# Optimization experiments

Measured on AMD Instinct MI355X. Metric: run time of the kernel, lower is better.

The kernel has to match this reference:

```python
import jax, jax.numpy as jnp
import numpy as np

N_NODES = 50000
N_EDGES = 800000
D_IN, D_HID, D_OUT = 128, 128, 256
EPS = 1e-12  # F.normalize eps


def _mean_aggr(h, src, dst, n):
    # scatter-mean of source features onto destination nodes
    msg_sum = jax.ops.segment_sum(h[src], dst, num_segments=n)
    deg = jax.ops.segment_sum(jnp.ones((src.shape[0],), h.dtype), dst, num_segments=n)
    return msg_sum / jnp.maximum(deg, 1.0)[:, None]


def _l2_normalize(h):
    # F.normalize(p=2, dim=1): divide by clamped L2 norm
    nrm = jnp.sqrt(jnp.sum(h * h, axis=1, keepdims=True))
    return h / jnp.maximum(nrm, EPS)


def setup_inputs() -> dict:
    key = jax.random.key(0)
    ks = jax.random.split(key, 8)
    x = jax.random.normal(ks[0], (N_NODES, D_IN), dtype=jnp.float32)
    edge_index = jax.random.randint(ks[1], (2, N_EDGES), 0, N_NODES, dtype=jnp.int64 if jax.config.read('jax_enable_x64') else jnp.int32)
    s = 1.0 / np.sqrt(D_IN)
    W1_l = jax.random.uniform(ks[2], (D_IN, D_HID), jnp.float32, -s, s)
    W1_r = jax.random.uniform(ks[3], (D_IN, D_HID), jnp.float32, -s, s)
    b1 = jnp.zeros((D_HID,), jnp.float32)
    s2 = 1.0 / np.sqrt(D_HID)
    W2_l = jax.random.uniform(ks[4], (D_HID, D_OUT), jnp.float32, -s2, s2)
    W2_r = jax.random.uniform(ks[5], (D_HID, D_OUT), jnp.float32, -s2, s2)
    b2 = jnp.zeros((D_OUT,), jnp.float32)
    return {"x": x, "edge_index": edge_index, "W1_l": W1_l, "W1_r": W1_r,
            "b1": b1, "W2_l": W2_l, "W2_r": W2_r, "b2": b2}


def reference(x, edge_index, W1_l, W1_r, b1, W2_l, W2_r, b2):
    src, dst = edge_index[0], edge_index[1]
    n = x.shape[0]
    # SAGEConv 1: lin_l(mean_aggr(x)) + lin_r(x) + bias
    h = _mean_aggr(x, src, dst, n) @ W1_l + x @ W1_r + b1
    # dropout is identity in eval mode
    h = _l2_normalize(jax.nn.sigmoid(h))
    # SAGEConv 2
    h = _mean_aggr(h, src, dst, n) @ W2_l + h @ W2_r + b2
    h = _l2_normalize(jax.nn.sigmoid(h))
    return jax.nn.log_softmax(h, axis=-1)
```

## Files before the change

### kernel.cpp

```cpp
#include <hip/hip_runtime.h>

#define NN 50000
#define NE 800000
#define NB 782
#define CAP 1536


__device__ __forceinline__ unsigned short f2bf(float f) {
    union { float f; unsigned u; } v; v.f = f;
    unsigned u = v.u;
    return (unsigned short)((u + 0x7fffu + ((u >> 16) & 1u)) >> 16);
}
__device__ __forceinline__ float bfu_lo(unsigned p) {
    union { unsigned u; float f; } v; v.u = p << 16; return v.f;
}
__device__ __forceinline__ float bfu_hi(unsigned p) {
    union { unsigned u; float f; } v; v.u = p & 0xffff0000u; return v.f;
}

typedef __bf16 bf16x8 __attribute__((ext_vector_type(8)));
typedef float f32x4 __attribute__((ext_vector_type(4)));
union U16 { uint4 u; bf16x8 v; };


__global__ __launch_bounds__(512) void binscatter_kernel(const int* __restrict__ src,
                                                         const int* __restrict__ dst,
                                                         int* __restrict__ bcnt,
                                                         unsigned* __restrict__ ebuf) {
    __shared__ int hist[NB];
    __shared__ int base[NB];
    const int BE = 8192;
    int tid = threadIdx.x;
    int e0 = blockIdx.x * BE;
    for (int i = tid; i < NB; i += 512) hist[i] = 0;
    __syncthreads();
    for (int i = tid; i < BE; i += 512) {
        int e = e0 + i;
        if (e < NE) atomicAdd(&hist[dst[e] >> 6], 1);
    }
    __syncthreads();
    for (int i = tid; i < NB; i += 512) {
        int c = hist[i];
        base[i] = c ? atomicAdd(&bcnt[i], c) : 0;
        hist[i] = 0;
    }
    __syncthreads();
    for (int i = tid; i < BE; i += 512) {
        int e = e0 + i;
        if (e < NE) {
            int d = dst[e], b = d >> 6;
            int slot = base[b] + atomicAdd(&hist[b], 1);
            if (slot < CAP)
                ebuf[(size_t)b * CAP + slot] = (unsigned)src[e] | ((unsigned)(d & 63) << 16);
        }
    }
}

__global__ __launch_bounds__(256) void csr_kernel(const int* __restrict__ bcnt,
                                                  const unsigned* __restrict__ ebuf,
                                                  int* __restrict__ rowptr,
                                                  int* __restrict__ col) {
    __shared__ int red[256];
    __shared__ int deg[64];
    __shared__ int cur[64];
    __shared__ int cbase_s;
    int b = blockIdx.x, tid = threadIdx.x;
    int s = 0;
    for (int i = tid; i < b; i += 256) s += bcnt[i];
    red[tid] = s;
    if (tid < 64) deg[tid] = 0;
    __syncthreads();
    for (int off = 128; off; off >>= 1) {
        if (tid < off) red[tid] += red[tid + off];
        __syncthreads();
    }
    if (tid == 0) cbase_s = red[0];
    __syncthreads();
    int cnt = bcnt[b], cbase = cbase_s;
    if (cnt > CAP) cnt = CAP;
    const unsigned* eb = ebuf + (size_t)b * CAP;
    for (int i = tid; i < cnt; i += 256) atomicAdd(&deg[(eb[i] >> 16) & 63], 1);
    __syncthreads();
    if (tid == 0) {
        int run = 0;
        for (int j = 0; j < 64; j++) { cur[j] = run; run += deg[j]; }
    }
    __syncthreads();
    int node = b * 64 + tid;
    if (tid < 64 && node < NN) rowptr[node] = cbase + cur[tid];
    if (b == NB - 1 && tid == 0) rowptr[NN] = NE;
    __syncthreads();
    for (int i = tid; i < cnt; i += 256) {
        unsigned e = eb[i];
        int pos = atomicAdd(&cur[(e >> 16) & 63], 1);
        col[cbase + pos] = (int)(e & 0xffffu);
    }
}


__global__ void cast_bf16_kernel(const float* __restrict__ in, unsigned short* __restrict__ outp,
                                 int n4) {
    int i = blockIdx.x * 256 + threadIdx.x;
    if (i < n4) {
        float4 f = ((const float4*)in)[i];
        ushort4 o;
        o.x = f2bf(f.x); o.y = f2bf(f.y); o.z = f2bf(f.z); o.w = f2bf(f.w);
        ((ushort4*)outp)[i] = o;
    }
}


template <int N>
__device__ __forceinline__ void pack_one(const float* __restrict__ Wl,
                                         const float* __restrict__ Wr,
                                         unsigned short* __restrict__ Wp, int t) {
    int lane = t & 63, c = t >> 6;
    int ks = c & 7, nt = c >> 3;
    int n = nt * 16 + (lane & 15);
    int kq = ks * 32 + (lane >> 4) * 8;
    unsigned short tmp[8];
#pragma unroll
    for (int j = 0; j < 8; j++) {
        int k = kq + j;
        float w = (k < 128) ? Wl[(size_t)k * N + n] : Wr[(size_t)(k - 128) * N + n];
        tmp[j] = f2bf(w);
    }
    ((ushort4*)Wp)[(size_t)c * 128 + lane * 2 + 0] = make_ushort4(tmp[0], tmp[1], tmp[2], tmp[3]);
    ((ushort4*)Wp)[(size_t)c * 128 + lane * 2 + 1] = make_ushort4(tmp[4], tmp[5], tmp[6], tmp[7]);
}

__global__ void pack_both_kernel(const float* __restrict__ W1l, const float* __restrict__ W1r,
                                 unsigned short* __restrict__ W1p,
                                 const float* __restrict__ W2l, const float* __restrict__ W2r,
                                 unsigned short* __restrict__ W2p) {
    int t = blockIdx.x * 256 + threadIdx.x;
    if (t < 8 * 8 * 64) pack_one<128>(W1l, W1r, W1p, t);
    else if (t < 8 * 8 * 64 + 16 * 8 * 64) pack_one<256>(W2l, W2r, W2p, t - 8 * 8 * 64);
}


__global__ void aggregate_bf_kernel(const int* __restrict__ rowptr, const int* __restrict__ col,
                                    const uint4* __restrict__ feat4,
                                    uint4* __restrict__ out4) {
    int wid = (blockIdx.x * blockDim.x + threadIdx.x) >> 6;
    int lane = threadIdx.x & 63;
    if (wid >= NN) return;
    int beg = rowptr[wid], end = rowptr[wid + 1];
    int g = lane >> 4, c16 = lane & 15;
    float acc[8];
#pragma unroll
    for (int j = 0; j < 8; j++) acc[j] = 0.f;
    for (int i = beg; i < end; i += 4) {
        int idx = i + g;
        if (idx < end) {
            int s = col[idx];
            uint4 v = feat4[(size_t)s * 16 + c16];
            acc[0] += bfu_lo(v.x); acc[1] += bfu_hi(v.x);
            acc[2] += bfu_lo(v.y); acc[3] += bfu_hi(v.y);
            acc[4] += bfu_lo(v.z); acc[5] += bfu_hi(v.z);
            acc[6] += bfu_lo(v.w); acc[7] += bfu_hi(v.w);
        }
    }
#pragma unroll
    for (int j = 0; j < 8; j++) {
        acc[j] += __shfl_xor(acc[j], 16);
        acc[j] += __shfl_xor(acc[j], 32);
    }
    if (g == 0) {
        float inv = (end > beg) ? 1.0f / (float)(end - beg) : 0.0f;
        uint4 o;
        o.x = (unsigned)f2bf(acc[0] * inv) | ((unsigned)f2bf(acc[1] * inv) << 16);
        o.y = (unsigned)f2bf(acc[2] * inv) | ((unsigned)f2bf(acc[3] * inv) << 16);
        o.z = (unsigned)f2bf(acc[4] * inv) | ((unsigned)f2bf(acc[5] * inv) << 16);
        o.w = (unsigned)f2bf(acc[6] * inv) | ((unsigned)f2bf(acc[7] * inv) << 16);
        out4[(size_t)wid * 16 + c16] = o;
    }
}


template <int N, bool FINAL>
__global__ __launch_bounds__(256) void gemm_mfma_kernel(
    const unsigned short* __restrict__ A0, const unsigned short* __restrict__ A1,
    const unsigned short* __restrict__ Wp, const float* __restrict__ bias,
    void* __restrict__ outp, int M) {
    const int NT = N / 16;
    int tid = threadIdx.x, wave = tid >> 6, lane = tid & 63;
    int quad = lane >> 4, col = lane & 15;
    int m_base = blockIdx.x * 64 + wave * 16;
    int row = m_base + col;
    int row_ld = row < M ? row : M - 1;

    bf16x8 a[8];
    const uint4* a0p = (const uint4*)(A0 + (size_t)row_ld * 128 + quad * 8);
    const uint4* a1p = (const uint4*)(A1 + (size_t)row_ld * 128 + quad * 8);
#pragma unroll
    for (int ks = 0; ks < 4; ks++) { U16 u; u.u = a0p[ks * 4]; a[ks] = u.v; }
#pragma unroll
    for (int ks = 0; ks < 4; ks++) { U16 u; u.u = a1p[ks * 4]; a[4 + ks] = u.v; }

    f32x4 acc[NT];
#pragma unroll
    for (int nt = 0; nt < NT; nt++) acc[nt] = (f32x4){0.f, 0.f, 0.f, 0.f};

    const uint4* wp = (const uint4*)Wp;
#pragma unroll
    for (int nt = 0; nt < NT; nt++) {
#pragma unroll
        for (int ks = 0; ks < 8; ks++) {
            U16 u; u.u = wp[(size_t)(nt * 8 + ks) * 64 + lane];
            acc[nt] = __builtin_amdgcn_mfma_f32_16x16x32_bf16(a[ks], u.v, acc[nt], 0, 0, 0);
        }
    }

    float ssq[4] = {0.f, 0.f, 0.f, 0.f};
#pragma unroll
    for (int nt = 0; nt < NT; nt++) {
        float bv = bias[nt * 16 + col];
#pragma unroll
        for (int r = 0; r < 4; r++) {
            float z = acc[nt][r] + bv;
            float s = 1.0f / (1.0f + __expf(-z));
            acc[nt][r] = s;
            ssq[r] += s * s;
        }
    }
#pragma unroll
    for (int r = 0; r < 4; r++) {
#pragma unroll
        for (int off = 1; off < 16; off <<= 1) ssq[r] += __shfl_xor(ssq[r], off, 16);
        float sc = 1.0f / fmaxf(sqrtf(ssq[r]), 1e-12f);
#pragma unroll
        for (int nt = 0; nt < NT; nt++) acc[nt][r] *= sc;
    }

    if (FINAL) {
#pragma unroll
        for (int r = 0; r < 4; r++) {
            float mx = -1e30f;
#pragma unroll
            for (int nt = 0; nt < NT; nt++) mx = fmaxf(mx, acc[nt][r]);
#pragma unroll
            for (int off = 1; off < 16; off <<= 1) mx = fmaxf(mx, __shfl_xor(mx, off, 16));
            float se = 0.f;
#pragma unroll
            for (int nt = 0; nt < NT; nt++) se += __expf(acc[nt][r] - mx);
#pragma unroll
            for (int off = 1; off < 16; off <<= 1) se += __shfl_xor(se, off, 16);
            float lse = mx + __logf(se);
#pragma unroll
            for (int nt = 0; nt < NT; nt++) acc[nt][r] -= lse;
        }
        float* op = (float*)outp;
#pragma unroll
        for (int r = 0; r < 4; r++) {
            int m = m_base + quad * 4 + r;
            if (m < M) {
#pragma unroll
                for (int nt = 0; nt < NT; nt++) op[(size_t)m * N + nt * 16 + col] = acc[nt][r];
            }
        }
    } else {
        unsigned short* op = (unsigned short*)outp;
#pragma unroll
        for (int r = 0; r < 4; r++) {
            int m = m_base + quad * 4 + r;
            if (m < M) {
#pragma unroll
                for (int nt = 0; nt < NT; nt++)
                    op[(size_t)m * N + nt * 16 + col] = f2bf(acc[nt][r]);
            }
        }
    }
}


extern "C" void kernel_launch(void* const* d_in, const int* in_sizes, int n_in,
                              void* d_out, int out_size, void* d_ws, size_t ws_size,
                              hipStream_t stream) {
    const float* x   = (const float*)d_in[0];
    const int*   ei  = (const int*)d_in[1];
    const float* W1l = (const float*)d_in[2];
    const float* W1r = (const float*)d_in[3];
    const float* b1  = (const float*)d_in[4];
    const float* W2l = (const float*)d_in[5];
    const float* W2r = (const float*)d_in[6];
    const float* b2  = (const float*)d_in[7];
    float* out = (float*)d_out;

    const int* src = ei;
    const int* dst = ei + NE;

    char* ws = (char*)d_ws;
    size_t off = 0;
    auto alloc = [&](size_t bytes) -> void* {
        void* p = ws + off;
        off += (bytes + 255) / 256 * 256;
        return p;
    };
    int* rowptr     = (int*)alloc((size_t)(NN + 1) * 4);
    int* col        = (int*)alloc((size_t)NE * 4);
    int* bcnt       = (int*)alloc((size_t)NB * 4);
    unsigned* ebuf  = (unsigned*)alloc((size_t)NB * CAP * 4);
    unsigned short* x_bf   = (unsigned short*)alloc((size_t)NN * 128 * 2);
    unsigned short* agg_bf = (unsigned short*)alloc((size_t)NN * 128 * 2);
    unsigned short* h1_bf  = (unsigned short*)alloc((size_t)NN * 128 * 2);
    unsigned short* W1p    = (unsigned short*)alloc((size_t)8 * 8 * 64 * 8 * 2);
    unsigned short* W2p    = (unsigned short*)alloc((size_t)16 * 8 * 64 * 8 * 2);

    hipMemsetAsync(bcnt, 0, (size_t)NB * 4, stream);
    binscatter_kernel<<<(NE + 8191) / 8192, 512, 0, stream>>>(src, dst, bcnt, ebuf);
    csr_kernel<<<NB, 256, 0, stream>>>(bcnt, ebuf, rowptr, col);

    cast_bf16_kernel<<<(NN * 128 / 4 + 255) / 256, 256, 0, stream>>>(x, x_bf, NN * 128 / 4);
    pack_both_kernel<<<(24 * 8 * 64 + 255) / 256, 256, 0, stream>>>(W1l, W1r, W1p, W2l, W2r, W2p);

    aggregate_bf_kernel<<<(NN + 3) / 4, 256, 0, stream>>>(rowptr, col, (const uint4*)x_bf,
                                                          (uint4*)agg_bf);
    gemm_mfma_kernel<128, false><<<(NN + 63) / 64, 256, 0, stream>>>(agg_bf, x_bf, W1p, b1,
                                                                     h1_bf, NN);
    aggregate_bf_kernel<<<(NN + 3) / 4, 256, 0, stream>>>(rowptr, col, (const uint4*)h1_bf,
                                                          (uint4*)agg_bf);
    gemm_mfma_kernel<256, true><<<(NN + 63) / 64, 256, 0, stream>>>(agg_bf, h1_bf, W2p, b2,
                                                                    out, NN);
}
```

Baseline: 253.4 us.

## Fuse neighbor aggregation into MFMA GEMM and merge prep kernels

```diff
diff --git a/kernel.cpp b/kernel.cpp
--- a/kernel.cpp
+++ b/kernel.cpp
@@ -23,29 +23,31 @@
 union U16 { uint4 u; bf16x8 v; };
 
 
-__global__ __launch_bounds__(512) void binscatter_kernel(const int* __restrict__ src,
-                                                         const int* __restrict__ dst,
-                                                         int* __restrict__ bcnt,
-                                                         unsigned* __restrict__ ebuf) {
+#define BS_BLOCKS ((NE + 8191) / 8192)
+#define CAST_BLOCKS ((NN * 128 / 4 + 255) / 256)
+#define PACK_BLOCKS ((24 * 8 * 64) / 256)
+
+__device__ void binscatter_job(const int* __restrict__ src, const int* __restrict__ dst,
+                               int* __restrict__ bcnt, unsigned* __restrict__ ebuf, int blk) {
     __shared__ int hist[NB];
     __shared__ int base[NB];
     const int BE = 8192;
     int tid = threadIdx.x;
-    int e0 = blockIdx.x * BE;
-    for (int i = tid; i < NB; i += 512) hist[i] = 0;
-    __syncthreads();
-    for (int i = tid; i < BE; i += 512) {
+    int e0 = blk * BE;
+    for (int i = tid; i < NB; i += 256) hist[i] = 0;
+    __syncthreads();
+    for (int i = tid; i < BE; i += 256) {
         int e = e0 + i;
         if (e < NE) atomicAdd(&hist[dst[e] >> 6], 1);
     }
     __syncthreads();
-    for (int i = tid; i < NB; i += 512) {
+    for (int i = tid; i < NB; i += 256) {
         int c = hist[i];
         base[i] = c ? atomicAdd(&bcnt[i], c) : 0;
         hist[i] = 0;
     }
     __syncthreads();
-    for (int i = tid; i < BE; i += 512) {
+    for (int i = tid; i < BE; i += 256) {
         int e = e0 + i;
         if (e < NE) {
             int d = dst[e], b = d >> 6;
@@ -55,6 +57,48 @@
         }
     }
 }
+
+template <int N>
+__device__ __forceinline__ void pack_one(const float* __restrict__ Wl,
+                                         const float* __restrict__ Wr,
+                                         unsigned short* __restrict__ Wp, int t) {
+    int lane = t & 63, c = t >> 6;
+    int ks = c & 7, nt = c >> 3;
+    int n = nt * 16 + (lane & 15);
+    int kq = ks * 32 + (lane >> 4) * 8;
+    unsigned short tmp[8];
+#pragma unroll
+    for (int j = 0; j < 8; j++) {
+        int k = kq + j;
+        float w = (k < 128) ? Wl[(size_t)k * N + n] : Wr[(size_t)(k - 128) * N + n];
+        tmp[j] = f2bf(w);
+    }
+    ((ushort4*)Wp)[(size_t)c * 128 + lane * 2 + 0] = make_ushort4(tmp[0], tmp[1], tmp[2], tmp[3]);
+    ((ushort4*)Wp)[(size_t)c * 128 + lane * 2 + 1] = make_ushort4(tmp[4], tmp[5], tmp[6], tmp[7]);
+}
+
+__global__ __launch_bounds__(256) void prep_kernel(
+    const int* __restrict__ src, const int* __restrict__ dst,
+    int* __restrict__ bcnt, unsigned* __restrict__ ebuf,
+    const float* __restrict__ x, unsigned short* __restrict__ x_bf,
+    const float* __restrict__ W1l, const float* __restrict__ W1r, unsigned short* __restrict__ W1p,
+    const float* __restrict__ W2l, const float* __restrict__ W2r, unsigned short* __restrict__ W2p) {
+    int b = blockIdx.x;
+    if (b < BS_BLOCKS) {
+        binscatter_job(src, dst, bcnt, ebuf, b);
+    } else if (b < BS_BLOCKS + CAST_BLOCKS) {
+        int i = (b - BS_BLOCKS) * 256 + threadIdx.x;
+        if (i < NN * 128 / 4) {
+            float4 f = ((const float4*)x)[i];
+            ((ushort4*)x_bf)[i] = make_ushort4(f2bf(f.x), f2bf(f.y), f2bf(f.z), f2bf(f.w));
+        }
+    } else {
+        int t = (b - BS_BLOCKS - CAST_BLOCKS) * 256 + threadIdx.x;
+        if (t < 8 * 8 * 64) pack_one<128>(W1l, W1r, W1p, t);
+        else if (t < 24 * 8 * 64) pack_one<256>(W2l, W2r, W2p, t - 8 * 8 * 64);
+    }
+}
+
 
 __global__ __launch_bounds__(256) void csr_kernel(const int* __restrict__ bcnt,
                                                   const unsigned* __restrict__ ebuf,
@@ -98,103 +142,65 @@
 }
 
 
-__global__ void cast_bf16_kernel(const float* __restrict__ in, unsigned short* __restrict__ outp,
-                                 int n4) {
-    int i = blockIdx.x * 256 + threadIdx.x;
-    if (i < n4) {
-        float4 f = ((const float4*)in)[i];
-        ushort4 o;
-        o.x = f2bf(f.x); o.y = f2bf(f.y); o.z = f2bf(f.z); o.w = f2bf(f.w);
-        ((ushort4*)outp)[i] = o;
-    }
-}
-
-
-template <int N>
-__device__ __forceinline__ void pack_one(const float* __restrict__ Wl,
-                                         const float* __restrict__ Wr,
-                                         unsigned short* __restrict__ Wp, int t) {
-    int lane = t & 63, c = t >> 6;
-    int ks = c & 7, nt = c >> 3;
-    int n = nt * 16 + (lane & 15);
-    int kq = ks * 32 + (lane >> 4) * 8;
-    unsigned short tmp[8];
-#pragma unroll
-    for (int j = 0; j < 8; j++) {
-        int k = kq + j;
-        float w = (k < 128) ? Wl[(size_t)k * N + n] : Wr[(size_t)(k - 128) * N + n];
-        tmp[j] = f2bf(w);
-    }
-    ((ushort4*)Wp)[(size_t)c * 128 + lane * 2 + 0] = make_ushort4(tmp[0], tmp[1], tmp[2], tmp[3]);
-    ((ushort4*)Wp)[(size_t)c * 128 + lane * 2 + 1] = make_ushort4(tmp[4], tmp[5], tmp[6], tmp[7]);
-}
-
-__global__ void pack_both_kernel(const float* __restrict__ W1l, const float* __restrict__ W1r,
-                                 unsigned short* __restrict__ W1p,
-                                 const float* __restrict__ W2l, const float* __restrict__ W2r,
-                                 unsigned short* __restrict__ W2p) {
-    int t = blockIdx.x * 256 + threadIdx.x;
-    if (t < 8 * 8 * 64) pack_one<128>(W1l, W1r, W1p, t);
-    else if (t < 8 * 8 * 64 + 16 * 8 * 64) pack_one<256>(W2l, W2r, W2p, t - 8 * 8 * 64);
-}
-
-
-__global__ void aggregate_bf_kernel(const int* __restrict__ rowptr, const int* __restrict__ col,
-                                    const uint4* __restrict__ feat4,
-                                    uint4* __restrict__ out4) {
-    int wid = (blockIdx.x * blockDim.x + threadIdx.x) >> 6;
-    int lane = threadIdx.x & 63;
-    if (wid >= NN) return;
-    int beg = rowptr[wid], end = rowptr[wid + 1];
+template <int N, bool FINAL>
+__global__ __launch_bounds__(256) void fused_layer_kernel(
+    const int* __restrict__ rowptr, const int* __restrict__ col,
+    const unsigned short* __restrict__ feat,
+    const unsigned short* __restrict__ Wp, const float* __restrict__ bias,
+    void* __restrict__ outp) {
+    const int NT = N / 16;
+    __shared__ uint4 sA[64 * 17];
+    int tid = threadIdx.x, wave = tid >> 6, lane = tid & 63;
     int g = lane >> 4, c16 = lane & 15;
-    float acc[8];
-#pragma unroll
-    for (int j = 0; j < 8; j++) acc[j] = 0.f;
-    for (int i = beg; i < end; i += 4) {
-        int idx = i + g;
-        if (idx < end) {
-            int s = col[idx];
-            uint4 v = feat4[(size_t)s * 16 + c16];
-            acc[0] += bfu_lo(v.x); acc[1] += bfu_hi(v.x);
-            acc[2] += bfu_lo(v.y); acc[3] += bfu_hi(v.y);
-            acc[4] += bfu_lo(v.z); acc[5] += bfu_hi(v.z);
-            acc[6] += bfu_lo(v.w); acc[7] += bfu_hi(v.w);
-        }
-    }
-#pragma unroll
-    for (int j = 0; j < 8; j++) {
-        acc[j] += __shfl_xor(acc[j], 16);
-        acc[j] += __shfl_xor(acc[j], 32);
-    }
-    if (g == 0) {
-        float inv = (end > beg) ? 1.0f / (float)(end - beg) : 0.0f;
-        uint4 o;
-        o.x = (unsigned)f2bf(acc[0] * inv) | ((unsigned)f2bf(acc[1] * inv) << 16);
-        o.y = (unsigned)f2bf(acc[2] * inv) | ((unsigned)f2bf(acc[3] * inv) << 16);
-        o.z = (unsigned)f2bf(acc[4] * inv) | ((unsigned)f2bf(acc[5] * inv) << 16);
-        o.w = (unsigned)f2bf(acc[6] * inv) | ((unsigned)f2bf(acc[7] * inv) << 16);
-        out4[(size_t)wid * 16 + c16] = o;
-    }
-}
-
-
-template <int N, bool FINAL>
-__global__ __launch_bounds__(256) void gemm_mfma_kernel(
-    const unsigned short* __restrict__ A0, const unsigned short* __restrict__ A1,
-    const unsigned short* __restrict__ Wp, const float* __restrict__ bias,
-    void* __restrict__ outp, int M) {
-    const int NT = N / 16;
-    int tid = threadIdx.x, wave = tid >> 6, lane = tid & 63;
-    int quad = lane >> 4, col = lane & 15;
+    const uint4* feat4 = (const uint4*)feat;
+
+    for (int t = 0; t < 16; t++) {
+        int node = blockIdx.x * 64 + wave * 16 + t;
+        if (node >= NN) break;
+        int beg = rowptr[node], end = rowptr[node + 1];
+        float ac[8];
+#pragma unroll
+        for (int j = 0; j < 8; j++) ac[j] = 0.f;
+        for (int i = beg; i < end; i += 4) {
+            int idx = i + g;
+            if (idx < end) {
+                int sn = col[idx];
+                uint4 v = feat4[(size_t)sn * 16 + c16];
+                ac[0] += bfu_lo(v.x); ac[1] += bfu_hi(v.x);
+                ac[2] += bfu_lo(v.y); ac[3] += bfu_hi(v.y);
+                ac[4] += bfu_lo(v.z); ac[5] += bfu_hi(v.z);
+                ac[6] += bfu_lo(v.w); ac[7] += bfu_hi(v.w);
+            }
+        }
+#pragma unroll
+        for (int j = 0; j < 8; j++) {
+            ac[j] += __shfl_xor(ac[j], 16);
+            ac[j] += __shfl_xor(ac[j], 32);
+        }
+        if (g == 0) {
+            float inv = (end > beg) ? 1.0f / (float)(end - beg) : 0.0f;
+            uint4 o;
+            o.x = (unsigned)f2bf(ac[0] * inv) | ((unsigned)f2bf(ac[1] * inv) << 16);
+            o.y = (unsigned)f2bf(ac[2] * inv) | ((unsigned)f2bf(ac[3] * inv) << 16);
+            o.z = (unsigned)f2bf(ac[4] * inv) | ((unsigned)f2bf(ac[5] * inv) << 16);
+            o.w = (unsigned)f2bf(ac[6] * inv) | ((unsigned)f2bf(ac[7] * inv) << 16);
+            sA[(wave * 16 + t) * 17 + c16] = o;
+        }
+    }
+    __syncthreads();
+
+    int quad = g, cl = c16;
     int m_base = blockIdx.x * 64 + wave * 16;
-    int row = m_base + col;
-    int row_ld = row < M ? row : M - 1;
+    int row = m_base + cl;
+    int row_ld = row < NN ? row : NN - 1;
 
     bf16x8 a[8];
-    const uint4* a0p = (const uint4*)(A0 + (size_t)row_ld * 128 + quad * 8);
-    const uint4* a1p = (const uint4*)(A1 + (size_t)row_ld * 128 + quad * 8);
-#pragma unroll
-    for (int ks = 0; ks < 4; ks++) { U16 u; u.u = a0p[ks * 4]; a[ks] = u.v; }
+#pragma unroll
+    for (int ks = 0; ks < 4; ks++) {
+        U16 u; u.u = sA[(wave * 16 + cl) * 17 + ks * 4 + quad];
+        a[ks] = u.v;
+    }
+    const uint4* a1p = (const uint4*)(feat + (size_t)row_ld * 128 + quad * 8);
 #pragma unroll
     for (int ks = 0; ks < 4; ks++) { U16 u; u.u = a1p[ks * 4]; a[4 + ks] = u.v; }
 
@@ -215,7 +221,7 @@
     float ssq[4] = {0.f, 0.f, 0.f, 0.f};
 #pragma unroll
     for (int nt = 0; nt < NT; nt++) {
-        float bv = bias[nt * 16 + col];
+        float bv = bias[nt * 16 + cl];
 #pragma unroll
         for (int r = 0; r < 4; r++) {
             float z = acc[nt][r] + bv;
@@ -254,9 +260,9 @@
 #pragma unroll
         for (int r = 0; r < 4; r++) {
             int m = m_base + quad * 4 + r;
-            if (m < M) {
-#pragma unroll
-                for (int nt = 0; nt < NT; nt++) op[(size_t)m * N + nt * 16 + col] = acc[nt][r];
+            if (m < NN) {
+#pragma unroll
+                for (int nt = 0; nt < NT; nt++) op[(size_t)m * N + nt * 16 + cl] = acc[nt][r];
             }
         }
     } else {
@@ -264,10 +270,10 @@
 #pragma unroll
         for (int r = 0; r < 4; r++) {
             int m = m_base + quad * 4 + r;
-            if (m < M) {
+            if (m < NN) {
 #pragma unroll
                 for (int nt = 0; nt < NT; nt++)
-                    op[(size_t)m * N + nt * 16 + col] = f2bf(acc[nt][r]);
+                    op[(size_t)m * N + nt * 16 + cl] = f2bf(acc[nt][r]);
             }
         }
     }
@@ -301,25 +307,17 @@
     int* col        = (int*)alloc((size_t)NE * 4);
     int* bcnt       = (int*)alloc((size_t)NB * 4);
     unsigned* ebuf  = (unsigned*)alloc((size_t)NB * CAP * 4);
-    unsigned short* x_bf   = (unsigned short*)alloc((size_t)NN * 128 * 2);
-    unsigned short* agg_bf = (unsigned short*)alloc((size_t)NN * 128 * 2);
-    unsigned short* h1_bf  = (unsigned short*)alloc((size_t)NN * 128 * 2);
-    unsigned short* W1p    = (unsigned short*)alloc((size_t)8 * 8 * 64 * 8 * 2);
-    unsigned short* W2p    = (unsigned short*)alloc((size_t)16 * 8 * 64 * 8 * 2);
+    unsigned short* x_bf  = (unsigned short*)alloc((size_t)NN * 128 * 2);
+    unsigned short* h1_bf = (unsigned short*)alloc((size_t)NN * 128 * 2);
+    unsigned short* W1p   = (unsigned short*)alloc((size_t)8 * 8 * 64 * 8 * 2);
+    unsigned short* W2p   = (unsigned short*)alloc((size_t)16 * 8 * 64 * 8 * 2);
 
     hipMemsetAsync(bcnt, 0, (size_t)NB * 4, stream);
-    binscatter_kernel<<<(NE + 8191) / 8192, 512, 0, stream>>>(src, dst, bcnt, ebuf);
+    prep_kernel<<<BS_BLOCKS + CAST_BLOCKS + PACK_BLOCKS, 256, 0, stream>>>(
+        src, dst, bcnt, ebuf, x, x_bf, W1l, W1r, W1p, W2l, W2r, W2p);
     csr_kernel<<<NB, 256, 0, stream>>>(bcnt, ebuf, rowptr, col);
-
-    cast_bf16_kernel<<<(NN * 128 / 4 + 255) / 256, 256, 0, stream>>>(x, x_bf, NN * 128 / 4);
-    pack_both_kernel<<<(24 * 8 * 64 + 255) / 256, 256, 0, stream>>>(W1l, W1r, W1p, W2l, W2r, W2p);
-
-    aggregate_bf_kernel<<<(NN + 3) / 4, 256, 0, stream>>>(rowptr, col, (const uint4*)x_bf,
-                                                          (uint4*)agg_bf);
-    gemm_mfma_kernel<128, false><<<(NN + 63) / 64, 256, 0, stream>>>(agg_bf, x_bf, W1p, b1,
-                                                                     h1_bf, NN);
-    aggregate_bf_kernel<<<(NN + 3) / 4, 256, 0, stream>>>(rowptr, col, (const uint4*)h1_bf,
-                                                          (uint4*)agg_bf);
-    gemm_mfma_kernel<256, true><<<(NN + 63) / 64, 256, 0, stream>>>(agg_bf, h1_bf, W2p, b2,
-                                                                    out, NN);
-}
+    fused_layer_kernel<128, false><<<(NN + 63) / 64, 256, 0, stream>>>(rowptr, col, x_bf, W1p,
+                                                                       b1, h1_bf);
+    fused_layer_kernel<256, true><<<(NN + 63) / 64, 256, 0, stream>>>(rowptr, col, h1_bf, W2p,
+                                                                      b2, out);
+}
```

After: 348.8 us. 1.38x slower.

## Merge prep kernels and split aggregation into column chunks over 16 neighbours

Applied to the files above, without the earlier changes.

```diff
diff --git a/kernel.cpp b/kernel.cpp
--- a/kernel.cpp
+++ b/kernel.cpp
@@ -23,29 +23,31 @@
 union U16 { uint4 u; bf16x8 v; };
 
 
-__global__ __launch_bounds__(512) void binscatter_kernel(const int* __restrict__ src,
-                                                         const int* __restrict__ dst,
-                                                         int* __restrict__ bcnt,
-                                                         unsigned* __restrict__ ebuf) {
+#define BS_BLOCKS ((NE + 8191) / 8192)
+#define CAST_BLOCKS ((NN * 128 / 4 + 255) / 256)
+#define PACK_BLOCKS ((24 * 8 * 64) / 256)
+
+__device__ void binscatter_job(const int* __restrict__ src, const int* __restrict__ dst,
+                               int* __restrict__ bcnt, unsigned* __restrict__ ebuf, int blk) {
     __shared__ int hist[NB];
     __shared__ int base[NB];
     const int BE = 8192;
     int tid = threadIdx.x;
-    int e0 = blockIdx.x * BE;
-    for (int i = tid; i < NB; i += 512) hist[i] = 0;
-    __syncthreads();
-    for (int i = tid; i < BE; i += 512) {
+    int e0 = blk * BE;
+    for (int i = tid; i < NB; i += 256) hist[i] = 0;
+    __syncthreads();
+    for (int i = tid; i < BE; i += 256) {
         int e = e0 + i;
         if (e < NE) atomicAdd(&hist[dst[e] >> 6], 1);
     }
     __syncthreads();
-    for (int i = tid; i < NB; i += 512) {
+    for (int i = tid; i < NB; i += 256) {
         int c = hist[i];
         base[i] = c ? atomicAdd(&bcnt[i], c) : 0;
         hist[i] = 0;
     }
     __syncthreads();
-    for (int i = tid; i < BE; i += 512) {
+    for (int i = tid; i < BE; i += 256) {
         int e = e0 + i;
         if (e < NE) {
             int d = dst[e], b = d >> 6;
@@ -55,6 +57,48 @@
         }
     }
 }
+
+template <int N>
+__device__ __forceinline__ void pack_one(const float* __restrict__ Wl,
+                                         const float* __restrict__ Wr,
+                                         unsigned short* __restrict__ Wp, int t) {
+    int lane = t & 63, c = t >> 6;
+    int ks = c & 7, nt = c >> 3;
+    int n = nt * 16 + (lane & 15);
+    int kq = ks * 32 + (lane >> 4) * 8;
+    unsigned short tmp[8];
+#pragma unroll
+    for (int j = 0; j < 8; j++) {
+        int k = kq + j;
+        float w = (k < 128) ? Wl[(size_t)k * N + n] : Wr[(size_t)(k - 128) * N + n];
+        tmp[j] = f2bf(w);
+    }
+    ((ushort4*)Wp)[(size_t)c * 128 + lane * 2 + 0] = make_ushort4(tmp[0], tmp[1], tmp[2], tmp[3]);
+    ((ushort4*)Wp)[(size_t)c * 128 + lane * 2 + 1] = make_ushort4(tmp[4], tmp[5], tmp[6], tmp[7]);
+}
+
+__global__ __launch_bounds__(256) void prep_kernel(
+    const int* __restrict__ src, const int* __restrict__ dst,
+    int* __restrict__ bcnt, unsigned* __restrict__ ebuf,
+    const float* __restrict__ x, unsigned short* __restrict__ x_bf,
+    const float* __restrict__ W1l, const float* __restrict__ W1r, unsigned short* __restrict__ W1p,
+    const float* __restrict__ W2l, const float* __restrict__ W2r, unsigned short* __restrict__ W2p) {
+    int b = blockIdx.x;
+    if (b < BS_BLOCKS) {
+        binscatter_job(src, dst, bcnt, ebuf, b);
+    } else if (b < BS_BLOCKS + CAST_BLOCKS) {
+        int i = (b - BS_BLOCKS) * 256 + threadIdx.x;
+        if (i < NN * 128 / 4) {
+            float4 f = ((const float4*)x)[i];
+            ((ushort4*)x_bf)[i] = make_ushort4(f2bf(f.x), f2bf(f.y), f2bf(f.z), f2bf(f.w));
+        }
+    } else {
+        int t = (b - BS_BLOCKS - CAST_BLOCKS) * 256 + threadIdx.x;
+        if (t < 8 * 8 * 64) pack_one<128>(W1l, W1r, W1p, t);
+        else if (t < 24 * 8 * 64) pack_one<256>(W2l, W2r, W2p, t - 8 * 8 * 64);
+    }
+}
+
 
 __global__ __launch_bounds__(256) void csr_kernel(const int* __restrict__ bcnt,
                                                   const unsigned* __restrict__ ebuf,
@@ -98,63 +142,23 @@
 }
 
 
-__global__ void cast_bf16_kernel(const float* __restrict__ in, unsigned short* __restrict__ outp,
-                                 int n4) {
-    int i = blockIdx.x * 256 + threadIdx.x;
-    if (i < n4) {
-        float4 f = ((const float4*)in)[i];
-        ushort4 o;
-        o.x = f2bf(f.x); o.y = f2bf(f.y); o.z = f2bf(f.z); o.w = f2bf(f.w);
-        ((ushort4*)outp)[i] = o;
-    }
-}
-
-
-template <int N>
-__device__ __forceinline__ void pack_one(const float* __restrict__ Wl,
-                                         const float* __restrict__ Wr,
-                                         unsigned short* __restrict__ Wp, int t) {
-    int lane = t & 63, c = t >> 6;
-    int ks = c & 7, nt = c >> 3;
-    int n = nt * 16 + (lane & 15);
-    int kq = ks * 32 + (lane >> 4) * 8;
-    unsigned short tmp[8];
-#pragma unroll
-    for (int j = 0; j < 8; j++) {
-        int k = kq + j;
-        float w = (k < 128) ? Wl[(size_t)k * N + n] : Wr[(size_t)(k - 128) * N + n];
-        tmp[j] = f2bf(w);
-    }
-    ((ushort4*)Wp)[(size_t)c * 128 + lane * 2 + 0] = make_ushort4(tmp[0], tmp[1], tmp[2], tmp[3]);
-    ((ushort4*)Wp)[(size_t)c * 128 + lane * 2 + 1] = make_ushort4(tmp[4], tmp[5], tmp[6], tmp[7]);
-}
-
-__global__ void pack_both_kernel(const float* __restrict__ W1l, const float* __restrict__ W1r,
-                                 unsigned short* __restrict__ W1p,
-                                 const float* __restrict__ W2l, const float* __restrict__ W2r,
-                                 unsigned short* __restrict__ W2p) {
-    int t = blockIdx.x * 256 + threadIdx.x;
-    if (t < 8 * 8 * 64) pack_one<128>(W1l, W1r, W1p, t);
-    else if (t < 8 * 8 * 64 + 16 * 8 * 64) pack_one<256>(W2l, W2r, W2p, t - 8 * 8 * 64);
-}
-
-
 __global__ void aggregate_bf_kernel(const int* __restrict__ rowptr, const int* __restrict__ col,
                                     const uint4* __restrict__ feat4,
                                     uint4* __restrict__ out4) {
-    int wid = (blockIdx.x * blockDim.x + threadIdx.x) >> 6;
+    int c = blockIdx.x / 12500;
+    int node = (blockIdx.x % 12500) * 4 + (threadIdx.x >> 6);
     int lane = threadIdx.x & 63;
-    if (wid >= NN) return;
-    int beg = rowptr[wid], end = rowptr[wid + 1];
-    int g = lane >> 4, c16 = lane & 15;
+    if (node >= NN) return;
+    int beg = rowptr[node], end = rowptr[node + 1];
+    int nb = lane >> 2, sub = lane & 3;
     float acc[8];
 #pragma unroll
     for (int j = 0; j < 8; j++) acc[j] = 0.f;
-    for (int i = beg; i < end; i += 4) {
-        int idx = i + g;
+    for (int i = beg; i < end; i += 16) {
+        int idx = i + nb;
         if (idx < end) {
             int s = col[idx];
-            uint4 v = feat4[(size_t)s * 16 + c16];
+            uint4 v = feat4[(size_t)s * 16 + c * 4 + sub];
             acc[0] += bfu_lo(v.x); acc[1] += bfu_hi(v.x);
             acc[2] += bfu_lo(v.y); acc[3] += bfu_hi(v.y);
             acc[4] += bfu_lo(v.z); acc[5] += bfu_hi(v.z);
@@ -163,17 +167,19 @@
     }
 #pragma unroll
     for (int j = 0; j < 8; j++) {
+        acc[j] += __shfl_xor(acc[j], 4);
+        acc[j] += __shfl_xor(acc[j], 8);
         acc[j] += __shfl_xor(acc[j], 16);
         acc[j] += __shfl_xor(acc[j], 32);
     }
-    if (g == 0) {
+    if (lane < 4) {
         float inv = (end > beg) ? 1.0f / (float)(end - beg) : 0.0f;
         uint4 o;
         o.x = (unsigned)f2bf(acc[0] * inv) | ((unsigned)f2bf(acc[1] * inv) << 16);
         o.y = (unsigned)f2bf(acc[2] * inv) | ((unsigned)f2bf(acc[3] * inv) << 16);
         o.z = (unsigned)f2bf(acc[4] * inv) | ((unsigned)f2bf(acc[5] * inv) << 16);
         o.w = (unsigned)f2bf(acc[6] * inv) | ((unsigned)f2bf(acc[7] * inv) << 16);
-        out4[(size_t)wid * 16 + c16] = o;
+        out4[(size_t)node * 16 + c * 4 + lane] = o;
     }
 }
 
@@ -308,18 +314,16 @@
     unsigned short* W2p    = (unsigned short*)alloc((size_t)16 * 8 * 64 * 8 * 2);
 
     hipMemsetAsync(bcnt, 0, (size_t)NB * 4, stream);
-    binscatter_kernel<<<(NE + 8191) / 8192, 512, 0, stream>>>(src, dst, bcnt, ebuf);
+    prep_kernel<<<BS_BLOCKS + CAST_BLOCKS + PACK_BLOCKS, 256, 0, stream>>>(
+        src, dst, bcnt, ebuf, x, x_bf, W1l, W1r, W1p, W2l, W2r, W2p);
     csr_kernel<<<NB, 256, 0, stream>>>(bcnt, ebuf, rowptr, col);
 
-    cast_bf16_kernel<<<(NN * 128 / 4 + 255) / 256, 256, 0, stream>>>(x, x_bf, NN * 128 / 4);
-    pack_both_kernel<<<(24 * 8 * 64 + 255) / 256, 256, 0, stream>>>(W1l, W1r, W1p, W2l, W2r, W2p);
-
-    aggregate_bf_kernel<<<(NN + 3) / 4, 256, 0, stream>>>(rowptr, col, (const uint4*)x_bf,
-                                                          (uint4*)agg_bf);
+    aggregate_bf_kernel<<<4 * 12500, 256, 0, stream>>>(rowptr, col, (const uint4*)x_bf,
+                                                       (uint4*)agg_bf);
     gemm_mfma_kernel<128, false><<<(NN + 63) / 64, 256, 0, stream>>>(agg_bf, x_bf, W1p, b1,
                                                                      h1_bf, NN);
-    aggregate_bf_kernel<<<(NN + 3) / 4, 256, 0, stream>>>(rowptr, col, (const uint4*)h1_bf,
-                                                          (uint4*)agg_bf);
+    aggregate_bf_kernel<<<4 * 12500, 256, 0, stream>>>(rowptr, col, (const uint4*)h1_bf,
+                                                       (uint4*)agg_bf);
     gemm_mfma_kernel<256, true><<<(NN + 63) / 64, 256, 0, stream>>>(agg_bf, h1_bf, W2p, b2,
                                                                     out, NN);
 }
```

After: 331.8 us. 1.31x slower.
